# Kernel tuning notes

Measured on AMD Instinct MI355X. Metric: run time of the kernel, lower is better.

## Reference

```python
import jax, jax.numpy as jnp
import numpy as np

N = 12000       # num nodes
E = 384000      # num edges (avg degree 32)
F_IN = 512      # num_feats
H = 64          # gnn_hid_dim (== anchor_dim)
C = 7           # num_cls
SIGMA = 1.0


def setup_inputs() -> dict:
    key = jax.random.key(0)
    ks = jax.random.split(key, 9)
    scale = lambda fan_in: 1.0 / np.sqrt(fan_in)
    return {
        "x": jax.random.normal(ks[0], (N, F_IN), dtype=jnp.float32),
        "W1": jax.random.normal(ks[1], (F_IN, H), dtype=jnp.float32) * scale(F_IN),
        "b1": jnp.zeros((H,), dtype=jnp.float32),
        "W2": jax.random.normal(ks[2], (H, H), dtype=jnp.float32) * scale(H),
        "b2": jnp.zeros((H,), dtype=jnp.float32),
        "aux": jax.random.normal(ks[3], (H,), dtype=jnp.float32),
        "clf_W": jax.random.normal(ks[4], (2 * H, C), dtype=jnp.float32) * scale(2 * H),
        "clf_b": jnp.zeros((C,), dtype=jnp.float32),
        "edge_index": jax.random.randint(ks[5], (2, E), 0, N, dtype=jnp.int64),
    }


def gcn_conv(x, W, b, src, dst, n):
    # GCNConv: D^{-1/2} (A + I) D^{-1/2} X W + b, with self-loops
    h = x @ W                                                   # [N, out]
    deg = jax.ops.segment_sum(jnp.ones(src.shape[0], h.dtype), dst,
                              num_segments=n) + 1.0             # +1 for self-loop
    inv_sqrt = jax.lax.rsqrt(deg)
    norm = inv_sqrt[src] * inv_sqrt[dst]                        # [E]
    agg = jax.ops.segment_sum(h[src] * norm[:, None], dst, num_segments=n)
    agg = agg + h / deg[:, None]                                # self-loop term (norm = 1/deg)
    return agg + b


def reference(x, W1, b1, W2, b2, aux, clf_W, clf_b, edge_index):
    src, dst = edge_index[0], edge_index[1]
    n = x.shape[0]
    h = jax.nn.relu(gcn_conv(x, W1, b1, src, dst, n))
    h = gcn_conv(h, W2, b2, src, dst, n)                        # [N, H]
    # kernel aggregate: pairwise Gaussian kernel on cosine scores
    a = aux / jnp.maximum(jnp.linalg.norm(aux), 1e-12)          # F.normalize
    hn = jnp.maximum(jnp.linalg.norm(h, axis=-1), 1e-8)         # cosine_similarity eps
    score = (h @ a) / hn                                        # [N]
    diff = score[None, :] - score[:, None]                      # [N, N]
    kappa = jnp.exp(-(diff * diff) / (SIGMA * SIGMA))           # [N, N]
    z = (kappa @ h) / jnp.sum(kappa, axis=1, keepdims=True)     # [N, H]
    return jnp.concatenate([h, z], axis=-1) @ clf_W + clf_b     # [N, C]
```

## Files before the change

### kernel.cpp

```cpp
#include <hip/hip_runtime.h>
#include <hip/hip_bf16.h>

#define N_NODES 12000
#define N_EDGES 384000
#define F_IN 512
#define H 64
#define C_CLS 7
#define KTERMS 16
#define PAD 96
#define CSTR 32
#define MOM_BLKS 192
#define NB 4
#define GEMM_BLKS 375
#define FILL_BLKS 256
#define XS_STR 68

__device__ __forceinline__ float wred_f(float x) {
    #pragma unroll
    for (int o = 32; o > 0; o >>= 1) x += __shfl_xor(x, o);
    return x;
}

__global__ __launch_bounds__(256) void init_k(int* __restrict__ cur,
                                              double* __restrict__ M,
                                              double* __restrict__ m0) {
    int i = blockIdx.x * 256 + threadIdx.x;
    if (i < N_NODES) cur[i * CSTR] = 0;
    if (i < KTERMS * 64) M[i] = 0.0;
    if (i < KTERMS) m0[i] = 0.0;
}

__global__ __launch_bounds__(256) void k1_gemm_fill(const float* __restrict__ x,
                                                    const float* __restrict__ W1,
                                                    const int* __restrict__ ei,
                                                    float* __restrict__ hbuf,
                                                    int* __restrict__ cur,
                                                    int* __restrict__ csrc) {
    const int b = blockIdx.x, t = threadIdx.x;
    if (b < GEMM_BLKS) {
        __shared__ float xs[32 * XS_STR];
        __shared__ float wsm[64 * 64];
        const int tx = t & 15, ty = t >> 4;
        const int i0 = b * 32;
        float acc[2][4] = {};
        for (int k0 = 0; k0 < F_IN; k0 += 64) {
            #pragma unroll
            for (int q = 0; q < 2; ++q) {
                int idx = t + q * 256;
                int row = idx >> 4, kg = idx & 15;
                *(float4*)(&xs[row * XS_STR + kg * 4]) =
                    *(const float4*)(x + (size_t)(i0 + row) * F_IN + k0 + kg * 4);
            }
            #pragma unroll
            for (int q = 0; q < 4; ++q) {
                int idx = t + q * 256;
                int r = idx >> 4, cg = idx & 15;
                *(float4*)(&wsm[r * 64 + cg * 4]) =
                    *(const float4*)(W1 + (size_t)(k0 + r) * H + cg * 4);
            }
            __syncthreads();
            #pragma unroll
            for (int kk0 = 0; kk0 < 64; kk0 += 4) {
                float4 a0 = *(const float4*)(&xs[(ty * 2 + 0) * XS_STR + kk0]);
                float4 a1 = *(const float4*)(&xs[(ty * 2 + 1) * XS_STR + kk0]);
                float4 b0 = *(const float4*)(&wsm[(kk0 + 0) * 64 + tx * 4]);
                float4 b1v = *(const float4*)(&wsm[(kk0 + 1) * 64 + tx * 4]);
                float4 b2v = *(const float4*)(&wsm[(kk0 + 2) * 64 + tx * 4]);
                float4 b3v = *(const float4*)(&wsm[(kk0 + 3) * 64 + tx * 4]);
                acc[0][0] += a0.x * b0.x;  acc[0][1] += a0.x * b0.y;  acc[0][2] += a0.x * b0.z;  acc[0][3] += a0.x * b0.w;
                acc[0][0] += a0.y * b1v.x; acc[0][1] += a0.y * b1v.y; acc[0][2] += a0.y * b1v.z; acc[0][3] += a0.y * b1v.w;
                acc[0][0] += a0.z * b2v.x; acc[0][1] += a0.z * b2v.y; acc[0][2] += a0.z * b2v.z; acc[0][3] += a0.z * b2v.w;
                acc[0][0] += a0.w * b3v.x; acc[0][1] += a0.w * b3v.y; acc[0][2] += a0.w * b3v.z; acc[0][3] += a0.w * b3v.w;
                acc[1][0] += a1.x * b0.x;  acc[1][1] += a1.x * b0.y;  acc[1][2] += a1.x * b0.z;  acc[1][3] += a1.x * b0.w;
                acc[1][0] += a1.y * b1v.x; acc[1][1] += a1.y * b1v.y; acc[1][2] += a1.y * b1v.z; acc[1][3] += a1.y * b1v.w;
                acc[1][0] += a1.z * b2v.x; acc[1][1] += a1.z * b2v.y; acc[1][2] += a1.z * b2v.z; acc[1][3] += a1.z * b2v.w;
                acc[1][0] += a1.w * b3v.x; acc[1][1] += a1.w * b3v.y; acc[1][2] += a1.w * b3v.z; acc[1][3] += a1.w * b3v.w;
            }
            __syncthreads();
        }
        #pragma unroll
        for (int r = 0; r < 2; ++r) {
            int row = i0 + ty * 2 + r;
            *(float4*)(hbuf + (size_t)row * H + tx * 4) =
                make_float4(acc[r][0], acc[r][1], acc[r][2], acc[r][3]);
        }
    } else {
        for (int e = (b - GEMM_BLKS) * 256 + t; e < N_EDGES; e += FILL_BLKS * 256) {
            int s = ei[e];
            int d = ei[N_EDGES + e];
            int pos = atomicAdd(&cur[d * CSTR], 1);
            if (pos < PAD) csrc[d * PAD + pos] = s;
        }
    }
}

__global__ __launch_bounds__(256) void invs_k(const int* __restrict__ cur,
                                              float* __restrict__ invs) {
    int i = blockIdx.x * 256 + threadIdx.x;
    if (i < N_NODES) invs[i] = rsqrtf((float)cur[i * CSTR] + 1.0f);
}

__global__ __launch_bounds__(256) void agg1_k(const float* __restrict__ hbuf,
                                              const float* __restrict__ b1,
                                              const int* __restrict__ cur,
                                              const int* __restrict__ csrc,
                                              const float* __restrict__ invs,
                                              float* __restrict__ h1) {
    __shared__ int2 sPair[NB * PAD];
    __shared__ int sDeg[NB];
    __shared__ float sIsd[NB];
    const int t = threadIdx.x, f = t & 63, w = t >> 6;
    const int base = blockIdx.x * NB;
    if (t < NB) {
        sDeg[t] = min(cur[(base + t) * CSTR], PAD);
        sIsd[t] = invs[base + t];
    }
    __syncthreads();
    for (int idx = t; idx < NB * PAD; idx += 256) {
        int n = idx / PAD, e = idx - n * PAD;
        if (e < sDeg[n]) {
            int s = csrc[(base + n) * PAD + e];
            sPair[idx] = make_int2(s, __float_as_int(invs[s]));
        }
    }
    __syncthreads();
    const int i = base + w;
    const int deg = sDeg[w];
    const float isd = sIsd[w];
    const int2* pp = sPair + w * PAD;
    float acc = 0.f;
    int e = 0;
    for (; e + 8 <= deg; e += 8) {
        int2 p0 = pp[e], p1 = pp[e+1], p2 = pp[e+2], p3 = pp[e+3];
        int2 p4 = pp[e+4], p5 = pp[e+5], p6 = pp[e+6], p7 = pp[e+7];
        acc += hbuf[p0.x * H + f] * __int_as_float(p0.y)
             + hbuf[p1.x * H + f] * __int_as_float(p1.y)
             + hbuf[p2.x * H + f] * __int_as_float(p2.y)
             + hbuf[p3.x * H + f] * __int_as_float(p3.y)
             + hbuf[p4.x * H + f] * __int_as_float(p4.y)
             + hbuf[p5.x * H + f] * __int_as_float(p5.y)
             + hbuf[p6.x * H + f] * __int_as_float(p6.y)
             + hbuf[p7.x * H + f] * __int_as_float(p7.y);
    }
    for (; e + 4 <= deg; e += 4) {
        int2 p0 = pp[e], p1 = pp[e+1], p2 = pp[e+2], p3 = pp[e+3];
        acc += hbuf[p0.x * H + f] * __int_as_float(p0.y)
             + hbuf[p1.x * H + f] * __int_as_float(p1.y)
             + hbuf[p2.x * H + f] * __int_as_float(p2.y)
             + hbuf[p3.x * H + f] * __int_as_float(p3.y);
    }
    for (; e < deg; ++e) {
        int2 p = pp[e];
        acc += hbuf[p.x * H + f] * __int_as_float(p.y);
    }
    float res = (acc + hbuf[i * H + f] * isd) * isd + b1[f];
    h1[i * H + f] = fmaxf(res, 0.f);
}

__global__ __launch_bounds__(256) void agg2_k(const float* __restrict__ h1,
                                              const float* __restrict__ W2,
                                              const float* __restrict__ b2,
                                              const float* __restrict__ aux,
                                              const int* __restrict__ cur,
                                              const int* __restrict__ csrc,
                                              const float* __restrict__ invs,
                                              float* __restrict__ h2,
                                              float* __restrict__ score) {
    __shared__ float w2s[64 * 64];
    __shared__ int2 sPair[NB * PAD];
    __shared__ int sDeg[NB];
    __shared__ float sIsd[NB];
    __shared__ float anorm[64];
    __shared__ float gsh[NB * 64];
    const int t = threadIdx.x, f = t & 63, w = t >> 6;
    const int base = blockIdx.x * NB;
    #pragma unroll
    for (int q = 0; q < 4; ++q) {
        int idx = t + q * 256;
        int r = idx >> 4, c4 = idx & 15;
        *(float4*)(&w2s[r * 64 + c4 * 4]) = *(const float4*)(W2 + r * H + c4 * 4);
    }
    if (t < NB) {
        sDeg[t] = min(cur[(base + t) * CSTR], PAD);
        sIsd[t] = invs[base + t];
    }
    if (t < 64) {
        float av = aux[t];
        anorm[t] = av * rsqrtf(fmaxf(wred_f(av * av), 1e-24f));
    }
    __syncthreads();
    for (int idx = t; idx < NB * PAD; idx += 256) {
        int n = idx / PAD, e = idx - n * PAD;
        if (e < sDeg[n]) {
            int s = csrc[(base + n) * PAD + e];
            sPair[idx] = make_int2(s, __float_as_int(invs[s]));
        }
    }
    __syncthreads();
    const int i = base + w;
    const int deg = sDeg[w];
    const float isd = sIsd[w];
    const int2* pp = sPair + w * PAD;
    float acc = 0.f;
    int e = 0;
    for (; e + 8 <= deg; e += 8) {
        int2 p0 = pp[e], p1 = pp[e+1], p2 = pp[e+2], p3 = pp[e+3];
        int2 p4 = pp[e+4], p5 = pp[e+5], p6 = pp[e+6], p7 = pp[e+7];
        acc += h1[p0.x * H + f] * __int_as_float(p0.y)
             + h1[p1.x * H + f] * __int_as_float(p1.y)
             + h1[p2.x * H + f] * __int_as_float(p2.y)
             + h1[p3.x * H + f] * __int_as_float(p3.y)
             + h1[p4.x * H + f] * __int_as_float(p4.y)
             + h1[p5.x * H + f] * __int_as_float(p5.y)
             + h1[p6.x * H + f] * __int_as_float(p6.y)
             + h1[p7.x * H + f] * __int_as_float(p7.y);
    }
    for (; e + 4 <= deg; e += 4) {
        int2 p0 = pp[e], p1 = pp[e+1], p2 = pp[e+2], p3 = pp[e+3];
        acc += h1[p0.x * H + f] * __int_as_float(p0.y)
             + h1[p1.x * H + f] * __int_as_float(p1.y)
             + h1[p2.x * H + f] * __int_as_float(p2.y)
             + h1[p3.x * H + f] * __int_as_float(p3.y);
    }
    for (; e < deg; ++e) {
        int2 p = pp[e];
        acc += h1[p.x * H + f] * __int_as_float(p.y);
    }
    float g = (acc + h1[i * H + f] * isd) * isd;
    gsh[w * 64 + f] = g;
    __builtin_amdgcn_wave_barrier();
    float hv = b2[f];
    #pragma unroll 16
    for (int k = 0; k < 64; ++k) hv += gsh[w * 64 + k] * w2s[k * 64 + f];
    h2[i * H + f] = hv;
    float dp = wred_f(hv * anorm[f]);
    float nn = wred_f(hv * hv);
    if (f == 0) score[i] = dp / fmaxf(sqrtf(nn), 1e-8f);
}

__global__ __launch_bounds__(256) void momden_k(const float* __restrict__ h2,
                                                const float* __restrict__ score,
                                                double* __restrict__ M,
                                                double* __restrict__ m0) {
    const int t = threadIdx.x, f = t & 63, g = t >> 6;
    float accM[KTERMS], accD[KTERMS];
    #pragma unroll
    for (int k = 0; k < KTERMS; ++k) { accM[k] = 0.f; accD[k] = 0.f; }
    for (int j = blockIdx.x * 4 + g; j < N_NODES; j += MOM_BLKS * 4) {
        float sj = score[j];
        float wj = expf(-sj * sj);
        float hv = h2[j * H + f];
        float tm = wj * hv, td = wj;
        #pragma unroll
        for (int k = 0; k < KTERMS; ++k) {
            accM[k] += tm; tm *= sj;
            accD[k] += td; td *= sj;
        }
    }
    __shared__ float Msh[4 * KTERMS * 64];
    __shared__ float Dsh[4 * KTERMS];
    #pragma unroll
    for (int k = 0; k < KTERMS; ++k) Msh[(g * KTERMS + k) * 64 + f] = accM[k];
    if (f == 0) {
        #pragma unroll
        for (int k = 0; k < KTERMS; ++k) Dsh[g * KTERMS + k] = accD[k];
    }
    __syncthreads();
    for (int idx = t; idx < KTERMS * 64; idx += 256) {
        int k = idx >> 6, ff = idx & 63;
        float sum = Msh[(0 * KTERMS + k) * 64 + ff] + Msh[(1 * KTERMS + k) * 64 + ff]
                  + Msh[(2 * KTERMS + k) * 64 + ff] + Msh[(3 * KTERMS + k) * 64 + ff];
        unsafeAtomicAdd(&M[idx], (double)sum);
    }
    if (t < KTERMS) {
        float sum = Dsh[t] + Dsh[KTERMS + t] + Dsh[2 * KTERMS + t] + Dsh[3 * KTERMS + t];
        unsafeAtomicAdd(&m0[t], (double)sum);
    }
}

__global__ __launch_bounds__(256) void final_k(const float* __restrict__ h2,
                                               const float* __restrict__ score,
                                               const double* __restrict__ M,
                                               const double* __restrict__ m0,
                                               const float* __restrict__ clfW,
                                               const float* __restrict__ clfb,
                                               float* __restrict__ out) {
    __shared__ float Ms[KTERMS * 64];
    __shared__ float m0s[KTERMS];
    __shared__ float cw[128 * C_CLS];
    __shared__ float cb[8];
    __shared__ float zh[4 * 128];
    const int t = threadIdx.x, f = t & 63, w = t >> 6;
    for (int idx = t; idx < KTERMS * 64; idx += 256) Ms[idx] = (float)M[idx];
    if (t < KTERMS) m0s[t] = (float)m0[t];
    for (int idx = t; idx < 128 * C_CLS; idx += 256) cw[idx] = clfW[idx];
    if (t < C_CLS) cb[t] = clfb[t];
    __syncthreads();
    const int base = blockIdx.x * 16;
    for (int q = 0; q < 4; ++q) {
        int i = base + q * 4 + w;
        float s = score[i];
        float c = expf(-s * s);
        float t2 = 2.f * s;
        float num = 0.f, den = 0.f;
        #pragma unroll
        for (int k = 0; k < KTERMS; ++k) {
            num += c * Ms[k * 64 + f];
            den += c * m0s[k];
            c *= t2 * (1.0f / (float)(k + 1));
        }
        zh[w * 128 + f] = h2[i * H + f];
        zh[w * 128 + 64 + f] = num / den;
        __builtin_amdgcn_wave_barrier();
        if (f < C_CLS) {
            float o = cb[f];
            #pragma unroll 8
            for (int u = 0; u < 128; ++u) o += zh[w * 128 + u] * cw[u * C_CLS + f];
            out[(size_t)i * C_CLS + f] = o;
        }
        __builtin_amdgcn_wave_barrier();
    }
}

extern "C" void kernel_launch(void* const* d_in, const int* in_sizes, int n_in,
                              void* d_out, int out_size, void* d_ws, size_t ws_size,
                              hipStream_t stream) {
    (void)in_sizes; (void)n_in; (void)out_size; (void)ws_size;
    const float* x    = (const float*)d_in[0];
    const float* W1   = (const float*)d_in[1];
    const float* b1   = (const float*)d_in[2];
    const float* W2   = (const float*)d_in[3];
    const float* b2   = (const float*)d_in[4];
    const float* aux  = (const float*)d_in[5];
    const float* clfW = (const float*)d_in[6];
    const float* clfb = (const float*)d_in[7];
    const int*   ei   = (const int*)d_in[8];
    float* out = (float*)d_out;
    char* ws = (char*)d_ws;

    float*  hbuf  = (float*)(ws + 0);
    float*  h1    = (float*)(ws + 3072000);
    float*  h2    = (float*)(ws + 6144000);
    float*  score = (float*)(ws + 9216000);
    float*  invs  = (float*)(ws + 9264000);
    int*    csrc  = (int*)  (ws + 9312000);
    int*    cur   = (int*)  (ws + 13920000);
    double* M     = (double*)(ws + 15456000);
    double* m0    = (double*)(ws + 15464192);

    init_k<<<47, 256, 0, stream>>>(cur, M, m0);
    k1_gemm_fill<<<GEMM_BLKS + FILL_BLKS, 256, 0, stream>>>(x, W1, ei, hbuf, cur, csrc);
    invs_k<<<47, 256, 0, stream>>>(cur, invs);
    agg1_k<<<N_NODES / NB, 256, 0, stream>>>(hbuf, b1, cur, csrc, invs, h1);
    agg2_k<<<N_NODES / NB, 256, 0, stream>>>(h1, W2, b2, aux, cur, csrc, invs, h2, score);
    momden_k<<<MOM_BLKS, 256, 0, stream>>>(h2, score, M, m0);
    final_k<<<750, 256, 0, stream>>>(h2, score, M, m0, clfW, clfb, out);
}
```

Measured before the change: 94.92 us.

## Drop invs kernel, recompute rsqrt inline; spread moment atomics over 8 copies

Removes the separate invs_k launch and computes the inverse-sqrt degree inline in both aggregation kernels from the cur counts. This trades one launch and a buffer for scattered reads of the strided cur array. It also raises the moment-kernel block count to 768 and splits the double-precision atomic accumulators into 8 replicas, reducing contention. final_k sums the 8 replicas when loading. init_k is enlarged so it zeroes all replicas.

```diff
diff --git a/kernel.cpp b/kernel.cpp
--- a/kernel.cpp
+++ b/kernel.cpp
@@ -9,7 +9,8 @@
 #define KTERMS 16
 #define PAD 96
 #define CSTR 32
-#define MOM_BLKS 192
+#define MOM_BLKS 768
+#define MSTR 1040
 #define NB 4
 #define GEMM_BLKS 375
 #define FILL_BLKS 256
@@ -22,12 +23,10 @@
 }
 
 __global__ __launch_bounds__(256) void init_k(int* __restrict__ cur,
-                                              double* __restrict__ M,
-                                              double* __restrict__ m0) {
+                                              double* __restrict__ M8) {
     int i = blockIdx.x * 256 + threadIdx.x;
     if (i < N_NODES) cur[i * CSTR] = 0;
-    if (i < KTERMS * 64) M[i] = 0.0;
-    if (i < KTERMS) m0[i] = 0.0;
+    if (i < 8 * MSTR) M8[i] = 0.0;
 }
 
 __global__ __launch_bounds__(256) void k1_gemm_fill(const float* __restrict__ x,
@@ -94,17 +93,10 @@
     }
 }
 
-__global__ __launch_bounds__(256) void invs_k(const int* __restrict__ cur,
-                                              float* __restrict__ invs) {
-    int i = blockIdx.x * 256 + threadIdx.x;
-    if (i < N_NODES) invs[i] = rsqrtf((float)cur[i * CSTR] + 1.0f);
-}
-
 __global__ __launch_bounds__(256) void agg1_k(const float* __restrict__ hbuf,
                                               const float* __restrict__ b1,
                                               const int* __restrict__ cur,
                                               const int* __restrict__ csrc,
-                                              const float* __restrict__ invs,
                                               float* __restrict__ h1) {
     __shared__ int2 sPair[NB * PAD];
     __shared__ int sDeg[NB];
@@ -112,15 +104,16 @@
     const int t = threadIdx.x, f = t & 63, w = t >> 6;
     const int base = blockIdx.x * NB;
     if (t < NB) {
-        sDeg[t] = min(cur[(base + t) * CSTR], PAD);
-        sIsd[t] = invs[base + t];
+        int d = cur[(base + t) * CSTR];
+        sDeg[t] = min(d, PAD);
+        sIsd[t] = rsqrtf((float)d + 1.f);
     }
     __syncthreads();
     for (int idx = t; idx < NB * PAD; idx += 256) {
         int n = idx / PAD, e = idx - n * PAD;
         if (e < sDeg[n]) {
             int s = csrc[(base + n) * PAD + e];
-            sPair[idx] = make_int2(s, __float_as_int(invs[s]));
+            sPair[idx] = make_int2(s, __float_as_int(rsqrtf((float)cur[s * CSTR] + 1.f)));
         }
     }
     __syncthreads();
@@ -163,7 +156,6 @@
                                               const float* __restrict__ aux,
                                               const int* __restrict__ cur,
                                               const int* __restrict__ csrc,
-                                              const float* __restrict__ invs,
                                               float* __restrict__ h2,
                                               float* __restrict__ score) {
     __shared__ float w2s[64 * 64];
@@ -181,8 +173,9 @@
         *(float4*)(&w2s[r * 64 + c4 * 4]) = *(const float4*)(W2 + r * H + c4 * 4);
     }
     if (t < NB) {
-        sDeg[t] = min(cur[(base + t) * CSTR], PAD);
-        sIsd[t] = invs[base + t];
+        int d = cur[(base + t) * CSTR];
+        sDeg[t] = min(d, PAD);
+        sIsd[t] = rsqrtf((float)d + 1.f);
     }
     if (t < 64) {
         float av = aux[t];
@@ -193,7 +186,7 @@
         int n = idx / PAD, e = idx - n * PAD;
         if (e < sDeg[n]) {
             int s = csrc[(base + n) * PAD + e];
-            sPair[idx] = make_int2(s, __float_as_int(invs[s]));
+            sPair[idx] = make_int2(s, __float_as_int(rsqrtf((float)cur[s * CSTR] + 1.f)));
         }
     }
     __syncthreads();
@@ -240,8 +233,7 @@
 
 __global__ __launch_bounds__(256) void momden_k(const float* __restrict__ h2,
                                                 const float* __restrict__ score,
-                                                double* __restrict__ M,
-                                                double* __restrict__ m0) {
+                                                double* __restrict__ M8) {
     const int t = threadIdx.x, f = t & 63, g = t >> 6;
     float accM[KTERMS], accD[KTERMS];
     #pragma unroll
@@ -266,22 +258,22 @@
         for (int k = 0; k < KTERMS; ++k) Dsh[g * KTERMS + k] = accD[k];
     }
     __syncthreads();
+    double* Mc = M8 + (size_t)(blockIdx.x & 7) * MSTR;
     for (int idx = t; idx < KTERMS * 64; idx += 256) {
         int k = idx >> 6, ff = idx & 63;
         float sum = Msh[(0 * KTERMS + k) * 64 + ff] + Msh[(1 * KTERMS + k) * 64 + ff]
                   + Msh[(2 * KTERMS + k) * 64 + ff] + Msh[(3 * KTERMS + k) * 64 + ff];
-        unsafeAtomicAdd(&M[idx], (double)sum);
+        unsafeAtomicAdd(&Mc[idx], (double)sum);
     }
     if (t < KTERMS) {
         float sum = Dsh[t] + Dsh[KTERMS + t] + Dsh[2 * KTERMS + t] + Dsh[3 * KTERMS + t];
-        unsafeAtomicAdd(&m0[t], (double)sum);
+        unsafeAtomicAdd(&Mc[1024 + t], (double)sum);
     }
 }
 
 __global__ __launch_bounds__(256) void final_k(const float* __restrict__ h2,
                                                const float* __restrict__ score,
-                                               const double* __restrict__ M,
-                                               const double* __restrict__ m0,
+                                               const double* __restrict__ M8,
                                                const float* __restrict__ clfW,
                                                const float* __restrict__ clfb,
                                                float* __restrict__ out) {
@@ -291,8 +283,18 @@
     __shared__ float cb[8];
     __shared__ float zh[4 * 128];
     const int t = threadIdx.x, f = t & 63, w = t >> 6;
-    for (int idx = t; idx < KTERMS * 64; idx += 256) Ms[idx] = (float)M[idx];
-    if (t < KTERMS) m0s[t] = (float)m0[t];
+    for (int idx = t; idx < KTERMS * 64; idx += 256) {
+        double s = 0.0;
+        #pragma unroll
+        for (int c = 0; c < 8; ++c) s += M8[(size_t)c * MSTR + idx];
+        Ms[idx] = (float)s;
+    }
+    if (t < KTERMS) {
+        double s = 0.0;
+        #pragma unroll
+        for (int c = 0; c < 8; ++c) s += M8[(size_t)c * MSTR + 1024 + t];
+        m0s[t] = (float)s;
+    }
     for (int idx = t; idx < 128 * C_CLS; idx += 256) cw[idx] = clfW[idx];
     if (t < C_CLS) cb[t] = clfb[t];
     __syncthreads();
@@ -342,17 +344,14 @@
     float*  h1    = (float*)(ws + 3072000);
     float*  h2    = (float*)(ws + 6144000);
     float*  score = (float*)(ws + 9216000);
-    float*  invs  = (float*)(ws + 9264000);
-    int*    csrc  = (int*)  (ws + 9312000);
-    int*    cur   = (int*)  (ws + 13920000);
-    double* M     = (double*)(ws + 15456000);
-    double* m0    = (double*)(ws + 15464192);
-
-    init_k<<<47, 256, 0, stream>>>(cur, M, m0);
+    int*    csrc  = (int*)  (ws + 9264000);
+    int*    cur   = (int*)  (ws + 13872000);
+    double* M8    = (double*)(ws + 15408000);
+
+    init_k<<<47, 256, 0, stream>>>(cur, M8);
     k1_gemm_fill<<<GEMM_BLKS + FILL_BLKS, 256, 0, stream>>>(x, W1, ei, hbuf, cur, csrc);
-    invs_k<<<47, 256, 0, stream>>>(cur, invs);
-    agg1_k<<<N_NODES / NB, 256, 0, stream>>>(hbuf, b1, cur, csrc, invs, h1);
-    agg2_k<<<N_NODES / NB, 256, 0, stream>>>(h1, W2, b2, aux, cur, csrc, invs, h2, score);
-    momden_k<<<MOM_BLKS, 256, 0, stream>>>(h2, score, M, m0);
-    final_k<<<750, 256, 0, stream>>>(h2, score, M, m0, clfW, clfb, out);
-}
+    agg1_k<<<N_NODES / NB, 256, 0, stream>>>(hbuf, b1, cur, csrc, h1);
+    agg2_k<<<N_NODES / NB, 256, 0, stream>>>(h1, W2, b2, aux, cur, csrc, h2, score);
+    momden_k<<<MOM_BLKS, 256, 0, stream>>>(h2, score, M8);
+    final_k<<<750, 256, 0, stream>>>(h2, score, M8, clfW, clfb, out);
+}
```

New measurement: 95.13 us. About the same (+0.2%).
